# Performance work log

Measured on AMD Instinct MI355X. Metric: run time of the kernel, lower is better.

Reference implementation:

```python
import jax, jax.numpy as jnp
import numpy as np

N = 50000      # nodes
E = 1600000    # edges (avg degree 32)
H = 2          # num_heads
F = 32         # att_feat
IN = 32        # in_feats (must equal att_feat, see w1(h_dst + g))
OUT = 32       # out_feats
NEG_SLOPE = 0.2


def setup_inputs() -> dict:
    key = jax.random.key(0)
    ks = jax.random.split(key, 11)
    s = 0.1  # param init scale
    return {
        "feat": jax.random.normal(ks[0], (N, IN), jnp.float32),
        "r_feat": jax.random.normal(ks[1], (E, H, F), jnp.float32),
        "src": jax.random.randint(ks[2], (E,), 0, N),
        "dst": jax.random.randint(ks[3], (E,), 0, N),
        "W1": jax.random.normal(ks[4], (IN, OUT), jnp.float32) * s,
        "b1": jnp.zeros((OUT,), jnp.float32),
        "W2s": jax.random.normal(ks[5], (IN, H * F), jnp.float32) * s,
        "b2s": jnp.zeros((H * F,), jnp.float32),
        "W2d": jax.random.normal(ks[6], (IN, H * F), jnp.float32) * s,
        "b2d": jnp.zeros((H * F,), jnp.float32),
        "attn": jax.random.normal(ks[7], (1, H, F), jnp.float32) * s,
    }


def reference(feat, r_feat, src, dst, W1, b1, W2s, b2s, W2d, b2d, attn):
    n = feat.shape[0]
    # projections (dropout = 0 -> identity)
    feat_src = (feat @ W2s + b2s).reshape(n, H, F)   # [N,H,F]
    feat_dst = (feat @ W2d + b2d).reshape(n, H, F)   # [N,H,F]
    en = feat_src[src]                                # [E,H,F] gather
    ev = feat_dst[dst]                                # [E,H,F] gather
    # u_add_v + leaky_relu, dot with attention vector
    e = jax.nn.leaky_relu(en + ev, negative_slope=NEG_SLOPE)
    e = jnp.sum(e * attn, axis=-1, keepdims=True)     # [E,H,1]
    # edge_softmax: softmax over incoming edges of each dst node
    m = jax.ops.segment_max(e, dst, num_segments=n)   # [N,H,1]
    m = jnp.where(jnp.isfinite(m), m, 0.0)            # zero in-degree -> -inf
    ee = jnp.exp(e - m[dst])                          # [E,H,1]
    denom = jax.ops.segment_sum(ee, dst, num_segments=n)
    alpha = ee / jnp.maximum(denom[dst], 1e-9)        # [E,H,1]
    # message: softmax over feature dim of (en * rr * alpha)
    msg = jax.nn.softmax(en * r_feat * alpha, axis=-1)  # [E,H,F]
    g_agg = jax.ops.segment_sum(msg, dst, num_segments=n)  # [N,H,F]
    g_sum = jnp.sum(g_agg, axis=1)                    # att_agg='sum' -> [N,F]
    rst = (feat + g_sum) @ W1 + b1                    # [N,OUT]
    return rst
```

## Files before the change

### kernel.cpp

```cpp
#include <hip/hip_runtime.h>

#define N_NODES 50000
#define E_EDGES 1600000
#define NHEAD 2
#define FDIM 32
#define HF 64
#define IN_F 32
#define OUT_F 32
#define CAPB 128

__device__ __forceinline__ int rl(int v, int l) { return __builtin_amdgcn_readlane(v, l); }

template<int CTRL>
__device__ __forceinline__ float dpp_add(float v) {
    int t = __builtin_amdgcn_update_dpp(0, __float_as_int(v), CTRL, 0xf, 0xf, true);
    return v + __int_as_float(t);
}
__device__ __forceinline__ float red4_sum(float v) {
    v = dpp_add<0xB1>(v);
    v = dpp_add<0x4E>(v);
    return v;
}
template<int PAT>
__device__ __forceinline__ float swz_add(float v) {
    return v + __int_as_float(__builtin_amdgcn_ds_swizzle(__float_as_int(v), PAT));
}
__device__ __forceinline__ float red64_sum(float v) {
    v = red4_sum(v);
    v = swz_add<0x101F>(v);
    v = swz_add<0x201F>(v);
    v = swz_add<0x401F>(v);
    v += __shfl_xor(v, 32, 64);
    return v;
}
__device__ __forceinline__ void load8(float* d, const float* __restrict__ p) {
    *(float4*)&d[0] = *(const float4*)&p[0];
    *(float4*)&d[4] = *(const float4*)&p[4];
}

__global__ void proj_kernel(const float* __restrict__ feat,
                            const float* __restrict__ W2s, const float* __restrict__ b2s,
                            const float* __restrict__ W2d, const float* __restrict__ b2d,
                            float* __restrict__ fsrc, float* __restrict__ fdst,
                            int* __restrict__ cur) {
    int idx = blockIdx.x * blockDim.x + threadIdx.x;
    int n = idx >> 6;
    int c = idx & 63;
    if (n >= N_NODES) return;
    if (c == 0) cur[n] = 0;
    const float* frow = feat + n * IN_F;
    float s = b2s[c];
    float d = b2d[c];
    #pragma unroll
    for (int k = 0; k < IN_F; ++k) {
        float fv = frow[k];
        s += fv * W2s[k * HF + c];
        d += fv * W2d[k * HF + c];
    }
    fsrc[n * HF + c] = s;
    fdst[n * HF + c] = d;
}

__global__ void scatter_kernel(const int4* __restrict__ src4, const int4* __restrict__ dst4,
                               int* __restrict__ cur, int2* __restrict__ pairs) {
    int i = blockIdx.x * blockDim.x + threadIdx.x;
    if (i * 4 < E_EDGES) {
        int4 s = src4[i];
        int4 d = dst4[i];
        int e = 4 * i;
        int p0 = atomicAdd(&cur[d.x], 1);
        if (p0 < CAPB) pairs[(size_t)d.x * CAPB + p0] = make_int2(s.x, e + 0);
        int p1 = atomicAdd(&cur[d.y], 1);
        if (p1 < CAPB) pairs[(size_t)d.y * CAPB + p1] = make_int2(s.y, e + 1);
        int p2 = atomicAdd(&cur[d.z], 1);
        if (p2 < CAPB) pairs[(size_t)d.z * CAPB + p2] = make_int2(s.z, e + 2);
        int p3 = atomicAdd(&cur[d.w], 1);
        if (p3 < CAPB) pairs[(size_t)d.w * CAPB + p3] = make_int2(s.w, e + 3);
    }
}

template<int NST>
__device__ __forceinline__ void agg_body(
        int deg, const int2* __restrict__ bucket,
        const float* __restrict__ fsrc, const float* __restrict__ rfeat,
        const float ev[8], const float aw[8], int hq, int eL, float g[8]) {
    int2 se[NST];
    float en[NST][8];
    #pragma unroll
    for (int j = 0; j < NST; ++j) {
        int idx = j * 16 + eL;
        se[j] = make_int2(0, 0);
        if (idx < deg) se[j] = bucket[idx];
        load8(en[j], fsrc + se[j].x * HF + hq);
    }
    float E[NST];
    float denp = 0.0f;
    #pragma unroll
    for (int j = 0; j < NST; ++j) {
        float acc = 0.0f;
        #pragma unroll
        for (int k = 0; k < 8; ++k) {
            float x = en[j][k] + ev[k];
            x = fmaxf(x, 0.2f * x);
            acc = fmaf(x, aw[k], acc);
        }
        float v = red4_sum(acc);
        E[j] = (j * 16 + eL < deg) ? __expf(v) : 0.0f;
        denp += E[j];
    }
    float den = red64_sum(denp) * 0.25f;
    float dinv = __builtin_amdgcn_rcpf(fmaxf(den, 1e-9f));
    #pragma unroll
    for (int j = 0; j < NST; ++j) {
        float r[8];
        load8(r, rfeat + (size_t)se[j].y * HF + hq);
        float a = E[j] * dinv;
        float p[8];
        float S = 0.0f;
        #pragma unroll
        for (int k = 0; k < 8; ++k) {
            p[k] = __expf(en[j][k] * r[k] * a);
            S += p[k];
        }
        S = red4_sum(S);
        float w = (j * 16 + eL < deg) ? __builtin_amdgcn_rcpf(S) : 0.0f;
        #pragma unroll
        for (int k = 0; k < 8; ++k) g[k] = fmaf(p[k], w, g[k]);
    }
}

__global__ __launch_bounds__(256) void agg_kernel(
        const int* __restrict__ cur, const int2* __restrict__ pairs,
        const float* __restrict__ fsrc, const float* __restrict__ fdst,
        const float* __restrict__ rfeat, const float* __restrict__ attn,
        const float* __restrict__ feat,
        const float* __restrict__ W1, const float* __restrict__ b1,
        float* __restrict__ out) {
    __shared__ __align__(16) float gpart[2][NHEAD][FDIM];
    int tid = threadIdx.x;
    int wib = tid >> 6;
    int nb = wib >> 1;
    int h = wib & 1;
    int n = blockIdx.x * 2 + nb;
    int lane = tid & 63;
    int eL = lane >> 2;
    int q = lane & 3;
    int deg = min(cur[n], CAPB);
    const int2* bucket = pairs + (size_t)n * CAPB;

    int hq = h * FDIM + q * 8;
    float ev[8], aw[8];
    load8(ev, fdst + n * HF + hq);
    load8(aw, attn + hq);

    float g[8] = {0, 0, 0, 0, 0, 0, 0, 0};
    if (deg <= 64) {
        int nst = (deg + 15) >> 4;
        if (nst <= 1)      agg_body<1>(deg, bucket, fsrc, rfeat, ev, aw, hq, eL, g);
        else if (nst == 2) agg_body<2>(deg, bucket, fsrc, rfeat, ev, aw, hq, eL, g);
        else if (nst == 3) agg_body<3>(deg, bucket, fsrc, rfeat, ev, aw, hq, eL, g);
        else               agg_body<4>(deg, bucket, fsrc, rfeat, ev, aw, hq, eL, g);
    } else {
        int nst = (deg + 15) >> 4;
        float denp = 0.0f;
        for (int j = 0; j < nst; ++j) {
            int idx = j * 16 + eL;
            int2 se = make_int2(0, 0);
            if (idx < deg) se = pairs[(size_t)n * CAPB + idx];
            float en[8];
            load8(en, fsrc + se.x * HF + hq);
            float acc = 0.0f;
            #pragma unroll
            for (int k = 0; k < 8; ++k) {
                float x = en[k] + ev[k];
                x = fmaxf(x, 0.2f * x);
                acc = fmaf(x, aw[k], acc);
            }
            float v = red4_sum(acc);
            denp += (idx < deg) ? __expf(v) : 0.0f;
        }
        float den = red64_sum(denp) * 0.25f;
        float dinv = __builtin_amdgcn_rcpf(fmaxf(den, 1e-9f));
        for (int j = 0; j < nst; ++j) {
            int idx = j * 16 + eL;
            int2 se = make_int2(0, 0);
            if (idx < deg) se = pairs[(size_t)n * CAPB + idx];
            float en[8], r[8], p[8];
            load8(en, fsrc + se.x * HF + hq);
            load8(r, rfeat + (size_t)se.y * HF + hq);
            float acc = 0.0f;
            #pragma unroll
            for (int k = 0; k < 8; ++k) {
                float x = en[k] + ev[k];
                x = fmaxf(x, 0.2f * x);
                acc = fmaf(x, aw[k], acc);
            }
            float v = red4_sum(acc);
            float a = ((idx < deg) ? __expf(v) : 0.0f) * dinv;
            float S = 0.0f;
            #pragma unroll
            for (int k = 0; k < 8; ++k) {
                p[k] = __expf(en[k] * r[k] * a);
                S += p[k];
            }
            S = red4_sum(S);
            float w = (idx < deg) ? __builtin_amdgcn_rcpf(S) : 0.0f;
            #pragma unroll
            for (int k = 0; k < 8; ++k) g[k] = fmaf(p[k], w, g[k]);
        }
    }

    #pragma unroll
    for (int k = 0; k < 8; ++k) {
        float v = g[k];
        v = swz_add<0x101F>(v);
        v = swz_add<0x201F>(v);
        v = swz_add<0x401F>(v);
        v += __shfl_xor(v, 32, 64);
        g[k] = v;
    }
    if (lane < 4) {
        *(float4*)&gpart[nb][h][lane * 8]     = make_float4(g[0], g[1], g[2], g[3]);
        *(float4*)&gpart[nb][h][lane * 8 + 4] = make_float4(g[4], g[5], g[6], g[7]);
    }
    __syncthreads();

    if (h == 0) {
        int f = lane & 31;
        float gs = gpart[nb][0][f] + gpart[nb][1][f];
        float x = feat[n * IN_F + f] + gs;
        float acc = b1[f];
        #pragma unroll
        for (int k = 0; k < 32; ++k) {
            float xk = __int_as_float(rl(__float_as_int(x), k));
            acc = fmaf(xk, W1[k * OUT_F + f], acc);
        }
        if (lane < 32) out[n * OUT_F + f] = acc;
    }
}

extern "C" void kernel_launch(void* const* d_in, const int* in_sizes, int n_in,
                              void* d_out, int out_size, void* d_ws, size_t ws_size,
                              hipStream_t stream) {
    const float* feat  = (const float*)d_in[0];
    const float* rfeat = (const float*)d_in[1];
    const int*   src   = (const int*)d_in[2];
    const int*   dst   = (const int*)d_in[3];
    const float* W1    = (const float*)d_in[4];
    const float* b1    = (const float*)d_in[5];
    const float* W2s   = (const float*)d_in[6];
    const float* b2s   = (const float*)d_in[7];
    const float* W2d   = (const float*)d_in[8];
    const float* b2d   = (const float*)d_in[9];
    const float* attn  = (const float*)d_in[10];
    float* out = (float*)d_out;

    float* fsrc = (float*)d_ws;
    float* fdst = fsrc + (size_t)N_NODES * HF;
    int*   cur  = (int*)(fdst + (size_t)N_NODES * HF);
    int2*  pairs = (int2*)(cur + N_NODES);

    const int BLK = 256;
    proj_kernel<<<(N_NODES * HF + BLK - 1) / BLK, BLK, 0, stream>>>(
        feat, W2s, b2s, W2d, b2d, fsrc, fdst, cur);
    scatter_kernel<<<(E_EDGES / 4 + BLK - 1) / BLK, BLK, 0, stream>>>(
        (const int4*)src, (const int4*)dst, cur, pairs);
    agg_kernel<<<N_NODES / 2, BLK, 0, stream>>>(
        cur, pairs, fsrc, fdst, rfeat, attn, feat, W1, b1, out);
}
```

Baseline: 272.9 us.

## Split each node's edges across two wave groups with shared-memory denominator reduction

The aggregation kernel now assigns one node per 256-thread block instead of two. The two wave pairs split that node's edge list (edges 0-31 and 32-63, with strided tails above 64), and the softmax denominator is combined through shared memory with an extra barrier. rfeat loads are issued before the barrier so they overlap the wait. This adds per-node parallelism and latency hiding for avg degree 32, at the cost of twice as many blocks, an extra sync, and only one wave doing the output matmul.

```diff
diff --git a/kernel.cpp b/kernel.cpp
--- a/kernel.cpp
+++ b/kernel.cpp
@@ -79,56 +79,6 @@
     }
 }
 
-template<int NST>
-__device__ __forceinline__ void agg_body(
-        int deg, const int2* __restrict__ bucket,
-        const float* __restrict__ fsrc, const float* __restrict__ rfeat,
-        const float ev[8], const float aw[8], int hq, int eL, float g[8]) {
-    int2 se[NST];
-    float en[NST][8];
-    #pragma unroll
-    for (int j = 0; j < NST; ++j) {
-        int idx = j * 16 + eL;
-        se[j] = make_int2(0, 0);
-        if (idx < deg) se[j] = bucket[idx];
-        load8(en[j], fsrc + se[j].x * HF + hq);
-    }
-    float E[NST];
-    float denp = 0.0f;
-    #pragma unroll
-    for (int j = 0; j < NST; ++j) {
-        float acc = 0.0f;
-        #pragma unroll
-        for (int k = 0; k < 8; ++k) {
-            float x = en[j][k] + ev[k];
-            x = fmaxf(x, 0.2f * x);
-            acc = fmaf(x, aw[k], acc);
-        }
-        float v = red4_sum(acc);
-        E[j] = (j * 16 + eL < deg) ? __expf(v) : 0.0f;
-        denp += E[j];
-    }
-    float den = red64_sum(denp) * 0.25f;
-    float dinv = __builtin_amdgcn_rcpf(fmaxf(den, 1e-9f));
-    #pragma unroll
-    for (int j = 0; j < NST; ++j) {
-        float r[8];
-        load8(r, rfeat + (size_t)se[j].y * HF + hq);
-        float a = E[j] * dinv;
-        float p[8];
-        float S = 0.0f;
-        #pragma unroll
-        for (int k = 0; k < 8; ++k) {
-            p[k] = __expf(en[j][k] * r[k] * a);
-            S += p[k];
-        }
-        S = red4_sum(S);
-        float w = (j * 16 + eL < deg) ? __builtin_amdgcn_rcpf(S) : 0.0f;
-        #pragma unroll
-        for (int k = 0; k < 8; ++k) g[k] = fmaf(p[k], w, g[k]);
-    }
-}
-
 __global__ __launch_bounds__(256) void agg_kernel(
         const int* __restrict__ cur, const int2* __restrict__ pairs,
         const float* __restrict__ fsrc, const float* __restrict__ fdst,
@@ -136,12 +86,13 @@
         const float* __restrict__ feat,
         const float* __restrict__ W1, const float* __restrict__ b1,
         float* __restrict__ out) {
+    __shared__ float denL[2][NHEAD];
     __shared__ __align__(16) float gpart[2][NHEAD][FDIM];
     int tid = threadIdx.x;
     int wib = tid >> 6;
-    int nb = wib >> 1;
-    int h = wib & 1;
-    int n = blockIdx.x * 2 + nb;
+    int h  = wib & 1;
+    int gr = wib >> 1;
+    int n = blockIdx.x;
     int lane = tid & 63;
     int eL = lane >> 2;
     int q = lane & 3;
@@ -153,45 +104,88 @@
     load8(ev, fdst + n * HF + hq);
     load8(aw, attn + hq);
 
-    float g[8] = {0, 0, 0, 0, 0, 0, 0, 0};
-    if (deg <= 64) {
-        int nst = (deg + 15) >> 4;
-        if (nst <= 1)      agg_body<1>(deg, bucket, fsrc, rfeat, ev, aw, hq, eL, g);
-        else if (nst == 2) agg_body<2>(deg, bucket, fsrc, rfeat, ev, aw, hq, eL, g);
-        else if (nst == 3) agg_body<3>(deg, bucket, fsrc, rfeat, ev, aw, hq, eL, g);
-        else               agg_body<4>(deg, bucket, fsrc, rfeat, ev, aw, hq, eL, g);
-    } else {
-        int nst = (deg + 15) >> 4;
-        float denp = 0.0f;
-        for (int j = 0; j < nst; ++j) {
-            int idx = j * 16 + eL;
-            int2 se = make_int2(0, 0);
-            if (idx < deg) se = pairs[(size_t)n * CAPB + idx];
-            float en[8];
-            load8(en, fsrc + se.x * HF + hq);
+    int2 se[2];
+    float en[2][8];
+    #pragma unroll
+    for (int j = 0; j < 2; ++j) {
+        int idx = gr * 32 + j * 16 + eL;
+        se[j] = make_int2(0, 0);
+        if (idx < deg) se[j] = bucket[idx];
+        load8(en[j], fsrc + se[j].x * HF + hq);
+    }
+    float E[2];
+    float denp = 0.0f;
+    #pragma unroll
+    for (int j = 0; j < 2; ++j) {
+        float acc = 0.0f;
+        #pragma unroll
+        for (int k = 0; k < 8; ++k) {
+            float x = en[j][k] + ev[k];
+            x = fmaxf(x, 0.2f * x);
+            acc = fmaf(x, aw[k], acc);
+        }
+        float v = red4_sum(acc);
+        E[j] = (gr * 32 + j * 16 + eL < deg) ? __expf(v) : 0.0f;
+        denp += E[j];
+    }
+    if (deg > 64) {
+        for (int b = 64 + gr * 16; b < deg; b += 32) {
+            int idx = b + eL;
+            int2 se2 = make_int2(0, 0);
+            if (idx < deg) se2 = bucket[idx];
+            float en2[8];
+            load8(en2, fsrc + se2.x * HF + hq);
             float acc = 0.0f;
             #pragma unroll
             for (int k = 0; k < 8; ++k) {
-                float x = en[k] + ev[k];
+                float x = en2[k] + ev[k];
                 x = fmaxf(x, 0.2f * x);
                 acc = fmaf(x, aw[k], acc);
             }
             float v = red4_sum(acc);
             denp += (idx < deg) ? __expf(v) : 0.0f;
         }
-        float den = red64_sum(denp) * 0.25f;
-        float dinv = __builtin_amdgcn_rcpf(fmaxf(den, 1e-9f));
-        for (int j = 0; j < nst; ++j) {
-            int idx = j * 16 + eL;
-            int2 se = make_int2(0, 0);
-            if (idx < deg) se = pairs[(size_t)n * CAPB + idx];
-            float en[8], r[8], p[8];
-            load8(en, fsrc + se.x * HF + hq);
-            load8(r, rfeat + (size_t)se.y * HF + hq);
+    }
+    float denw = red64_sum(denp) * 0.25f;
+    if (lane == 0) denL[gr][h] = denw;
+
+    float r[2][8];
+    #pragma unroll
+    for (int j = 0; j < 2; ++j)
+        load8(r[j], rfeat + (size_t)se[j].y * HF + hq);
+
+    __syncthreads();
+    float den = denL[0][h] + denL[1][h];
+    float dinv = __builtin_amdgcn_rcpf(fmaxf(den, 1e-9f));
+
+    float g[8] = {0, 0, 0, 0, 0, 0, 0, 0};
+    #pragma unroll
+    for (int j = 0; j < 2; ++j) {
+        float a = E[j] * dinv;
+        float p[8];
+        float S = 0.0f;
+        #pragma unroll
+        for (int k = 0; k < 8; ++k) {
+            p[k] = __expf(en[j][k] * r[j][k] * a);
+            S += p[k];
+        }
+        S = red4_sum(S);
+        float w = (gr * 32 + j * 16 + eL < deg) ? __builtin_amdgcn_rcpf(S) : 0.0f;
+        #pragma unroll
+        for (int k = 0; k < 8; ++k) g[k] = fmaf(p[k], w, g[k]);
+    }
+    if (deg > 64) {
+        for (int b = 64 + gr * 16; b < deg; b += 32) {
+            int idx = b + eL;
+            int2 se2 = make_int2(0, 0);
+            if (idx < deg) se2 = bucket[idx];
+            float en2[8], r2[8], p[8];
+            load8(en2, fsrc + se2.x * HF + hq);
+            load8(r2, rfeat + (size_t)se2.y * HF + hq);
             float acc = 0.0f;
             #pragma unroll
             for (int k = 0; k < 8; ++k) {
-                float x = en[k] + ev[k];
+                float x = en2[k] + ev[k];
                 x = fmaxf(x, 0.2f * x);
                 acc = fmaf(x, aw[k], acc);
             }
@@ -200,7 +194,7 @@
             float S = 0.0f;
             #pragma unroll
             for (int k = 0; k < 8; ++k) {
-                p[k] = __expf(en[k] * r[k] * a);
+                p[k] = __expf(en2[k] * r2[k] * a);
                 S += p[k];
             }
             S = red4_sum(S);
@@ -220,14 +214,14 @@
         g[k] = v;
     }
     if (lane < 4) {
-        *(float4*)&gpart[nb][h][lane * 8]     = make_float4(g[0], g[1], g[2], g[3]);
-        *(float4*)&gpart[nb][h][lane * 8 + 4] = make_float4(g[4], g[5], g[6], g[7]);
+        *(float4*)&gpart[gr][h][lane * 8]     = make_float4(g[0], g[1], g[2], g[3]);
+        *(float4*)&gpart[gr][h][lane * 8 + 4] = make_float4(g[4], g[5], g[6], g[7]);
     }
     __syncthreads();
 
-    if (h == 0) {
+    if (wib == 0) {
         int f = lane & 31;
-        float gs = gpart[nb][0][f] + gpart[nb][1][f];
+        float gs = (gpart[0][0][f] + gpart[0][1][f]) + (gpart[1][0][f] + gpart[1][1][f]);
         float x = feat[n * IN_F + f] + gs;
         float acc = b1[f];
         #pragma unroll
@@ -265,6 +259,6 @@
         feat, W2s, b2s, W2d, b2d, fsrc, fdst, cur);
     scatter_kernel<<<(E_EDGES / 4 + BLK - 1) / BLK, BLK, 0, stream>>>(
         (const int4*)src, (const int4*)dst, cur, pairs);
-    agg_kernel<<<N_NODES / 2, BLK, 0, stream>>>(
+    agg_kernel<<<N_NODES, BLK, 0, stream>>>(
         cur, pairs, fsrc, fdst, rfeat, attn, feat, W1, b1, out);
 }
```

Measured after the change: 285.0 us. +4.4%, slower.

## Store source projections as bf16 and prefetch edge features before softmax

Applied to the files above, without the earlier changes.

Source-node projections are now written as bf16 and unpacked to fp32 when they are gathered, which halves the bytes of the random per-edge gather from fsrc. The rfeat loads in the small-degree path are also issued up front, right after the fsrc gathers, so their latency overlaps the attention-score computation. This costs extra registers and bf16 rounding error on en, which feeds both the attention scores and the message exponent.

```diff
diff --git a/kernel.cpp b/kernel.cpp
--- a/kernel.cpp
+++ b/kernel.cpp
@@ -37,11 +37,23 @@
     *(float4*)&d[0] = *(const float4*)&p[0];
     *(float4*)&d[4] = *(const float4*)&p[4];
 }
+__device__ __forceinline__ void load8bf(float* d, const unsigned short* __restrict__ p) {
+    uint4 u = *(const uint4*)p;
+    d[0] = __uint_as_float(u.x << 16);  d[1] = __uint_as_float(u.x & 0xffff0000u);
+    d[2] = __uint_as_float(u.y << 16);  d[3] = __uint_as_float(u.y & 0xffff0000u);
+    d[4] = __uint_as_float(u.z << 16);  d[5] = __uint_as_float(u.z & 0xffff0000u);
+    d[6] = __uint_as_float(u.w << 16);  d[7] = __uint_as_float(u.w & 0xffff0000u);
+}
+__device__ __forceinline__ unsigned short f2bf(float f) {
+    unsigned int u = __float_as_uint(f);
+    u += 0x7fffu + ((u >> 16) & 1u);
+    return (unsigned short)(u >> 16);
+}
 
 __global__ void proj_kernel(const float* __restrict__ feat,
                             const float* __restrict__ W2s, const float* __restrict__ b2s,
                             const float* __restrict__ W2d, const float* __restrict__ b2d,
-                            float* __restrict__ fsrc, float* __restrict__ fdst,
+                            unsigned short* __restrict__ fsrc, float* __restrict__ fdst,
                             int* __restrict__ cur) {
     int idx = blockIdx.x * blockDim.x + threadIdx.x;
     int n = idx >> 6;
@@ -57,7 +69,7 @@
         s += fv * W2s[k * HF + c];
         d += fv * W2d[k * HF + c];
     }
-    fsrc[n * HF + c] = s;
+    fsrc[n * HF + c] = f2bf(s);
     fdst[n * HF + c] = d;
 }
 
@@ -82,17 +94,21 @@
 template<int NST>
 __device__ __forceinline__ void agg_body(
         int deg, const int2* __restrict__ bucket,
-        const float* __restrict__ fsrc, const float* __restrict__ rfeat,
+        const unsigned short* __restrict__ fsrc, const float* __restrict__ rfeat,
         const float ev[8], const float aw[8], int hq, int eL, float g[8]) {
     int2 se[NST];
-    float en[NST][8];
+    float en[NST][8], r[NST][8];
     #pragma unroll
     for (int j = 0; j < NST; ++j) {
         int idx = j * 16 + eL;
         se[j] = make_int2(0, 0);
         if (idx < deg) se[j] = bucket[idx];
-        load8(en[j], fsrc + se[j].x * HF + hq);
-    }
+        load8bf(en[j], fsrc + se[j].x * HF + hq);
+    }
+    #pragma unroll
+    for (int j = 0; j < NST; ++j)
+        load8(r[j], rfeat + (size_t)se[j].y * HF + hq);
+
     float E[NST];
     float denp = 0.0f;
     #pragma unroll
@@ -112,14 +128,12 @@
     float dinv = __builtin_amdgcn_rcpf(fmaxf(den, 1e-9f));
     #pragma unroll
     for (int j = 0; j < NST; ++j) {
-        float r[8];
-        load8(r, rfeat + (size_t)se[j].y * HF + hq);
         float a = E[j] * dinv;
         float p[8];
         float S = 0.0f;
         #pragma unroll
         for (int k = 0; k < 8; ++k) {
-            p[k] = __expf(en[j][k] * r[k] * a);
+            p[k] = __expf(en[j][k] * r[j][k] * a);
             S += p[k];
         }
         S = red4_sum(S);
@@ -131,7 +145,7 @@
 
 __global__ __launch_bounds__(256) void agg_kernel(
         const int* __restrict__ cur, const int2* __restrict__ pairs,
-        const float* __restrict__ fsrc, const float* __restrict__ fdst,
+        const unsigned short* __restrict__ fsrc, const float* __restrict__ fdst,
         const float* __restrict__ rfeat, const float* __restrict__ attn,
         const float* __restrict__ feat,
         const float* __restrict__ W1, const float* __restrict__ b1,
@@ -168,7 +182,7 @@
             int2 se = make_int2(0, 0);
             if (idx < deg) se = pairs[(size_t)n * CAPB + idx];
             float en[8];
-            load8(en, fsrc + se.x * HF + hq);
+            load8bf(en, fsrc + se.x * HF + hq);
             float acc = 0.0f;
             #pragma unroll
             for (int k = 0; k < 8; ++k) {
@@ -186,7 +200,7 @@
             int2 se = make_int2(0, 0);
             if (idx < deg) se = pairs[(size_t)n * CAPB + idx];
             float en[8], r[8], p[8];
-            load8(en, fsrc + se.x * HF + hq);
+            load8bf(en, fsrc + se.x * HF + hq);
             load8(r, rfeat + (size_t)se.y * HF + hq);
             float acc = 0.0f;
             #pragma unroll
@@ -255,8 +269,8 @@
     const float* attn  = (const float*)d_in[10];
     float* out = (float*)d_out;
 
-    float* fsrc = (float*)d_ws;
-    float* fdst = fsrc + (size_t)N_NODES * HF;
+    unsigned short* fsrc = (unsigned short*)d_ws;
+    float* fdst = (float*)(fsrc + (size_t)N_NODES * HF);
     int*   cur  = (int*)(fdst + (size_t)N_NODES * HF);
     int2*  pairs = (int2*)(cur + N_NODES);
 
```

Result: faster. 264.6 us, median of 2 (-3.1%).
